# Performance work log

Hardware: AMD Instinct MI355X
Metric: run time of the kernel (lower is better)

The kernel has to match this reference:

```python
import jax, jax.numpy as jnp
import numpy as np

B, T, D = 2, 2048, 2048
N, K, H = 16, 8, 128            # heads, kv heads, head_dim
SOFT_CAP = 50.0
WINDOW = 1024
SCALE = H ** -0.5               # query_pre_attn_scalar
ROPE_BASE = 10000.0
ROPE_SCALE = 1.0
K_MASK = -2.3819763e+38


def rms_norm(x, scale, eps=1e-6):
    var = jnp.mean(jnp.square(x), axis=-1, keepdims=True)
    return x * jax.lax.rsqrt(var + eps) * (1.0 + scale)


def apply_rope(x, positions):
    # x: [B,T,heads,H]; positions: [B,T] int
    head_dim = x.shape[-1]
    fraction = 2.0 * jnp.arange(head_dim // 2, dtype=jnp.float32) / head_dim
    timescale = ROPE_BASE ** fraction                      # [H/2]
    sinusoid = positions[..., None].astype(jnp.float32) / timescale  # [B,T,H/2]
    sinusoid = sinusoid[..., None, :] / ROPE_SCALE          # [B,T,1,H/2]
    sin, cos = jnp.sin(sinusoid), jnp.cos(sinusoid)
    first, second = jnp.split(x, 2, axis=-1)
    return jnp.concatenate([first * cos - second * sin,
                            second * cos + first * sin], axis=-1)


def setup_inputs() -> dict:
    key = jax.random.key(0)
    ks = jax.random.split(key, 6)
    x = jax.random.normal(ks[0], (B, T, D), jnp.float32)
    q_w = jax.random.normal(ks[1], (N, D, H), jnp.float32) * (D ** -0.5)
    kv_w = jax.random.normal(ks[2], (2, K, D, H), jnp.float32) * (D ** -0.5)
    o_w = jax.random.normal(ks[3], (N, H, D), jnp.float32) * ((N * H) ** -0.5)
    qnorm_scale = 0.1 * jax.random.normal(ks[4], (H,), jnp.float32)
    knorm_scale = 0.1 * jax.random.normal(ks[5], (H,), jnp.float32)
    segment_pos = jnp.broadcast_to(jnp.arange(T, dtype=jnp.int32), (B, T))
    attn_mask = jnp.broadcast_to(jnp.tril(jnp.ones((T, T), dtype=bool)), (B, T, T))
    return {"x": x, "q_w": q_w, "kv_w": kv_w, "o_w": o_w,
            "qnorm_scale": qnorm_scale, "knorm_scale": knorm_scale,
            "segment_pos": segment_pos, "attn_mask": attn_mask}


def reference(x, q_w, kv_w, o_w, qnorm_scale, knorm_scale, segment_pos, attn_mask):
    # projections
    q = jnp.einsum('BTD,NDH->BTNH', x, q_w)            # [B,T,N,H]
    k = jnp.einsum('BSD,KDH->BSKH', x, kv_w[0])        # [B,T,K,H]
    v = jnp.einsum('BSD,KDH->BSKH', x, kv_w[1])
    # QK RMSNorm, then RoPE, then query scaling (matches source order)
    q = apply_rope(rms_norm(q, qnorm_scale), segment_pos) * SCALE
    k = apply_rope(rms_norm(k, knorm_scale), segment_pos)
    # GQA: regroup query heads per kv head
    G = N // K
    qg = q.reshape(B, T, K, G, H)
    logits = jnp.einsum('BTKGH,BSKH->BTKGS', qg, k).reshape(B, T, N, T)
    # logit soft cap
    logits = jnp.tanh(logits / SOFT_CAP) * SOFT_CAP
    # sliding window mask combined with causal attn_mask
    pos_q = segment_pos[:, :, None]
    pos_k = segment_pos[:, None, :]
    sliding = (pos_k > pos_q - WINDOW) & (pos_k < pos_q + WINDOW)
    mask = attn_mask & sliding                          # [B,T,S]
    padded = jnp.where(mask[:, :, None, :], logits, K_MASK)
    probs = jax.nn.softmax(padded, axis=-1).astype(k.dtype)
    enc = jnp.einsum('BTKGS,BSKH->BTKGH',
                     probs.reshape(B, T, K, G, T), v).reshape(B, T, N, H)
    return jnp.einsum('BTNH,NHD->BTD', enc, o_w)
```

## Files before the change

kernel.cpp:

```cpp
#include <hip/hip_runtime.h>
#include <stdint.h>

#define BB 2
#define TT 2048
#define DD 2048
#define NHD 16
#define KVH 8
#define HD 128
#define JC 4096
#define WIN 1024
#define SCALE_Q 0.08838834764831845f

typedef __attribute__((ext_vector_type(8))) short bf16x8;
typedef __attribute__((ext_vector_type(8))) unsigned short us8;
typedef __attribute__((ext_vector_type(4))) unsigned short us4;
typedef __attribute__((ext_vector_type(4))) float f32x4;
typedef __attribute__((ext_vector_type(16))) float f32x16;
typedef __attribute__((ext_vector_type(4))) unsigned int u32x4;

#define GAS __attribute__((address_space(1)))
#define LAS __attribute__((address_space(3)))

__device__ __forceinline__ unsigned short f2bf(float f) {
  unsigned u = __float_as_uint(f);
  u += 0x7FFFu + ((u >> 16) & 1u);
  return (unsigned short)(u >> 16);
}
__device__ __forceinline__ float bf2f(unsigned short u) {
  return __uint_as_float(((unsigned)u) << 16);
}

__device__ __forceinline__ void gload16(const void* g, void* l) {
  __builtin_amdgcn_global_load_lds((const GAS unsigned int*)g, (LAS unsigned int*)l, 16, 0, 0);
}

#define VMCNT(n) asm volatile("s_waitcnt vmcnt(" #n ")" ::: "memory")

__global__ void __launch_bounds__(256) k_pre(
    const float4* __restrict__ x4, us4* __restrict__ xb,
    const float* __restrict__ qw, const float* __restrict__ kvw,
    const float* __restrict__ ow, unsigned short* __restrict__ Wt,
    unsigned short* __restrict__ Wt_o) {
  __shared__ float tile[32][33];
  int id = blockIdx.x;
  int tid = threadIdx.x;
  if (id < 8192) {
    int i = id * 256 + tid;
    float4 v = x4[i];
    us4 o;
    o[0] = f2bf(v.x); o[1] = f2bf(v.y); o[2] = f2bf(v.z); o[3] = f2bf(v.w);
    xb[i] = o;
    return;
  }
  const float* ib;
  unsigned short* ob;
  int ldin, c0, r0;
  int t = id - 8192;
  if (t < 8192) {
    int bx = t & 3, by = (t >> 2) & 63, z = t >> 8;
    ib = (z < 16) ? qw + (long)z * 2048 * 128 : kvw + (long)(z - 16) * 2048 * 128;
    ob = Wt + (long)z * 128 * 2048;
    ldin = 128;
    c0 = bx * 32; r0 = by * 32;
  } else {
    int u = t - 8192;
    ib = ow; ob = Wt_o; ldin = 2048;
    c0 = (u & 63) * 32; r0 = (u >> 6) * 32;
  }
  int tx = tid & 31, ty = tid >> 5;
#pragma unroll
  for (int i = 0; i < 4; i++)
    tile[ty + i * 8][tx] = ib[(long)(r0 + ty + i * 8) * ldin + c0 + tx];
  __syncthreads();
#pragma unroll
  for (int i = 0; i < 4; i++)
    ob[(long)(c0 + ty + i * 8) * 2048 + r0 + tx] = f2bf(tile[tx][ty + i * 8]);
}

template <bool BF16OUT>
__global__ void __launch_bounds__(512, 2) k_gemm8p(
    const unsigned short* __restrict__ A, const unsigned short* __restrict__ Bt,
    void* __restrict__ Cv, int Nn, int nby) {
  constexpr int KD = 2048;
  constexpr int NT = KD / 64;
  __shared__ short lds[2 * 4 * 8192];

  int tid = threadIdx.x, lane = tid & 63, w = tid >> 6;
  int wm = w >> 2, wn = w & 3;
  int id = blockIdx.x;
  int cpx = gridDim.x >> 3;
  id = (id & 7) * cpx + (id >> 3);
  int m0 = (id / nby) * 256, n0 = (id % nby) * 256;

  int srow = tid >> 3;
  int scol = ((tid & 7) ^ ((tid >> 3) & 7)) * 8;
  const unsigned short* gA = A + (long)(m0 + srow) * KD + scol;
  const unsigned short* gB = Bt + (long)(n0 + srow) * KD + scol;
  int wrow = w * 8 * 64;

  auto STG = [&](int p, int ko, int r) {
    const unsigned short* gsrc = (r < 2) ? gA + (long)(r * 128) * KD + ko
                                         : gB + (long)((r - 2) * 128) * KD + ko;
    short* dst = &lds[p * 32768 + r * 8192 + wrow];
#pragma unroll
    for (int i = 0; i < 2; ++i)
      gload16(gsrc + (long)(i * 64) * KD, dst + i * 4096);
  };

  int c0 = ((lane >> 4) ^ (lane & 7)) * 8;
  int abase = wm * 8192 + (lane & 15) * 64;
  int bbase = 16384 + (wn >> 1) * 8192 + ((wn & 1) * 64 + (lane & 15)) * 64;

  f32x4 acc[8][4] = {};
#pragma unroll
  for (int r = 0; r < 4; ++r) STG(0, 0, r);
  STG(1, 64, 2);
  STG(1, 64, 3);
  VMCNT(4);
  __builtin_amdgcn_s_barrier();

  bf16x8 bf[4][2];
  for (int t = 0; t < NT; ++t) {
    const short* bp = &lds[(t & 1) * 32768];
    int sb1 = (t + 1) & 1, sb2 = t & 1;
    int ko1 = (t + 1) * 64, ko2 = (t + 2) * 64;
    bool s1 = (t + 1) < NT, s2 = (t + 2) < NT;
#pragma unroll
    for (int q = 0; q < 4; ++q) {
      bf16x8 af[2][2];
#pragma unroll
      for (int m2 = 0; m2 < 2; ++m2)
#pragma unroll
        for (int kk = 0; kk < 2; ++kk)
          af[m2][kk] = *(const bf16x8*)&bp[abase + (q * 2 + m2) * 16 * 64 + (c0 ^ (kk * 32))];
      if (q == 0) {
#pragma unroll
        for (int ni = 0; ni < 4; ++ni)
#pragma unroll
          for (int kk = 0; kk < 2; ++kk)
            bf[ni][kk] = *(const bf16x8*)&bp[bbase + ni * 16 * 64 + (c0 ^ (kk * 32))];
      }
      if (q == 0) { if (s1) STG(sb1, ko1, 0); }
      else if (q == 1) { if (s1) STG(sb1, ko1, 1); }
      else if (q == 2) { if (s2) STG(sb2, ko2, 2); }
      else {
        if (s2) { STG(sb2, ko2, 3); VMCNT(4); }
        else if (s1) VMCNT(0);
      }
      __builtin_amdgcn_s_barrier();
      asm volatile("s_waitcnt lgkmcnt(0)" ::: "memory");
      __builtin_amdgcn_sched_barrier(0);
      __builtin_amdgcn_s_setprio(1);
#pragma unroll
      for (int m2 = 0; m2 < 2; ++m2)
#pragma unroll
        for (int ni = 0; ni < 4; ++ni)
#pragma unroll
          for (int kk = 0; kk < 2; ++kk)
            acc[q * 2 + m2][ni] = __builtin_amdgcn_mfma_f32_16x16x32_bf16(
                af[m2][kk], bf[ni][kk], acc[q * 2 + m2][ni], 0, 0, 0);
      __builtin_amdgcn_s_setprio(0);
      __builtin_amdgcn_s_barrier();
    }
  }

#pragma unroll
  for (int mi = 0; mi < 8; mi++)
#pragma unroll
    for (int ni = 0; ni < 4; ni++)
#pragma unroll
      for (int r = 0; r < 4; r++) {
        int row = m0 + wm * 128 + mi * 16 + (lane >> 4) * 4 + r;
        int col = n0 + wn * 64 + ni * 16 + (lane & 15);
        if constexpr (BF16OUT)
          ((unsigned short*)Cv)[(long)row * Nn + col] = f2bf(acc[mi][ni][r]);
        else
          ((float*)Cv)[(long)row * Nn + col] = acc[mi][ni][r];
      }
}

template <int BM, int BN, int NWN, int THREADS, int NBUF, bool BF16OUT>
__global__ void __launch_bounds__(THREADS, 2) k_gemm9(
    const unsigned short* __restrict__ A, const unsigned short* __restrict__ Bt,
    void* __restrict__ Cv, int M, int Nn, int nby) {
  constexpr int KD = 2048;
  constexpr int NT = KD / 32;
  constexpr int ROWS = BM + BN;
  constexpr int RPI = THREADS / 4;
  constexpr int IA = BM / RPI;
  constexpr int IPT = ROWS / RPI;
  constexpr int MT = BM / 32;
  constexpr int MT2 = MT / 2;
  __shared__ short lds[NBUF][ROWS * 32];

  int tid = threadIdx.x, lane = tid & 63, w = tid >> 6;
  int wm = w / NWN, wn = w % NWN;
  int id = blockIdx.x;
  int cpx = gridDim.x >> 3;
  id = (id & 7) * cpx + (id >> 3);
  int m0 = (id / nby) * BM, n0 = (id % nby) * BN;

  int srow = tid >> 2;
  int scol = ((tid & 3) ^ ((tid >> 3) & 3)) * 8;
  const unsigned short* gA = A + (long)(m0 + srow) * KD + scol;
  const unsigned short* gB = Bt + (long)(n0 + srow) * KD + scol;

  auto STG = [&](int p, int ko, int j) {
    if (j < IA)
      gload16(gA + (long)j * RPI * KD + ko, &lds[p][(j * RPI + w * 16) * 32]);
    else
      gload16(gB + (long)(j - IA) * RPI * KD + ko,
              &lds[p][(BM + (j - IA) * RPI + w * 16) * 32]);
  };

  int frag = (lane & 15) * 32 + (((lane >> 4) ^ ((lane >> 1) & 3)) * 8);
  int abase = wm * (BM / 2) * 32 + frag;
  int bbase = (BM + wn * 64) * 32 + frag;

  f32x4 acc[MT][4] = {};
#pragma unroll
  for (int tt = 0; tt < NBUF - 1; ++tt)
#pragma unroll
    for (int j = 0; j < IPT; ++j) STG(tt, tt * 32, j);
  {
    constexpr int PW = IPT * (NBUF - 2);
    if constexpr (PW >= 8)      VMCNT(8);
    else if constexpr (PW == 6) VMCNT(6);
    else if constexpr (PW == 4) VMCNT(4);
    else                        VMCNT(0);
  }
  __builtin_amdgcn_s_barrier();

  int buf = 0, sp = NBUF - 1;
  for (int t = 0; t < NT; ++t) {
    const short* bufp = lds[buf];
    bool st = (t + NBUF - 1) < NT;
    int ko = (t + NBUF - 1) * 32;
    bf16x8 bfr[4], af[MT2];
#pragma unroll
    for (int ni = 0; ni < 4; ++ni)
      bfr[ni] = *(const bf16x8*)&bufp[bbase + ni * 16 * 32];
#pragma unroll
    for (int mi = 0; mi < MT2; ++mi)
      af[mi] = *(const bf16x8*)&bufp[abase + mi * 16 * 32];
    if (st) {
#pragma unroll
      for (int j = 0; j < IPT / 2; ++j) STG(sp, ko, j);
    }
    __builtin_amdgcn_s_barrier();
    asm volatile("s_waitcnt lgkmcnt(0)" ::: "memory");
    __builtin_amdgcn_sched_barrier(0);
    __builtin_amdgcn_s_setprio(1);
#pragma unroll
    for (int mi = 0; mi < MT2; ++mi)
#pragma unroll
      for (int ni = 0; ni < 4; ++ni)
        acc[mi][ni] = __builtin_amdgcn_mfma_f32_16x16x32_bf16(af[mi], bfr[ni], acc[mi][ni], 0, 0, 0);
    __builtin_amdgcn_s_setprio(0);
    __builtin_amdgcn_s_barrier();
    bf16x8 af2[MT2];
#pragma unroll
    for (int mi = 0; mi < MT2; ++mi)
      af2[mi] = *(const bf16x8*)&bufp[abase + (MT2 + mi) * 16 * 32];
    if (st) {
#pragma unroll
      for (int j = IPT / 2; j < IPT; ++j) STG(sp, ko, j);
    }
    {
      int rem = NT - 2 - t;
      if (rem > NBUF - 2) rem = NBUF - 2;
      if (rem == 2) {
        if constexpr (IPT == 4) VMCNT(8); else VMCNT(12);
      } else if (rem == 1) {
        if constexpr (IPT == 4) VMCNT(4); else VMCNT(6);
      } else if (rem == 0) {
        VMCNT(0);
      }
    }
    __builtin_amdgcn_s_barrier();
    asm volatile("s_waitcnt lgkmcnt(0)" ::: "memory");
    __builtin_amdgcn_sched_barrier(0);
    __builtin_amdgcn_s_setprio(1);
#pragma unroll
    for (int mi = 0; mi < MT2; ++mi)
#pragma unroll
      for (int ni = 0; ni < 4; ++ni)
        acc[MT2 + mi][ni] = __builtin_amdgcn_mfma_f32_16x16x32_bf16(af2[mi], bfr[ni], acc[MT2 + mi][ni], 0, 0, 0);
    __builtin_amdgcn_s_setprio(0);
    __builtin_amdgcn_s_barrier();
    buf = (buf == NBUF - 1) ? 0 : buf + 1;
    sp = (sp == NBUF - 1) ? 0 : sp + 1;
  }

#pragma unroll
  for (int mi = 0; mi < MT; mi++)
#pragma unroll
    for (int ni = 0; ni < 4; ni++)
#pragma unroll
      for (int r = 0; r < 4; r++) {
        int row = m0 + wm * (BM / 2) + mi * 16 + (lane >> 4) * 4 + r;
        int col = n0 + wn * 64 + ni * 16 + (lane & 15);
        if constexpr (BF16OUT)
          ((unsigned short*)Cv)[(long)row * Nn + col] = f2bf(acc[mi][ni][r]);
        else
          ((float*)Cv)[(long)row * Nn + col] = acc[mi][ni][r];
      }
}

__global__ void __launch_bounds__(256) k_post(
    const unsigned short* __restrict__ qkv, const float* __restrict__ qns,
    const float* __restrict__ kns, unsigned short* __restrict__ qb,
    unsigned short* __restrict__ kb, unsigned short* __restrict__ vbT) {
  int id = blockIdx.x;
  int tid = threadIdx.x;
  if (id < 24576) {
    int wid = tid >> 6, lane = tid & 63;
    long r = (long)id * 4 + wid;
    int b = (int)(r / (TT * 24));
    int rem = (int)(r % (TT * 24));
    int t = rem / 24, hd = rem % 24;
    const unsigned short* row = qkv + (long)(b * TT + t) * JC + (hd < 16 ? hd * HD : 2048 + (hd - 16) * HD);
    float f0 = bf2f(row[lane]), f1 = bf2f(row[lane + 64]);
    float ss = f0 * f0 + f1 * f1;
#pragma unroll
    for (int m = 1; m < 64; m <<= 1) ss += __shfl_xor(ss, m, 64);
    float rinv = rsqrtf(ss * (1.0f / 128.0f) + 1e-6f);
    const float* sc = (hd < 16) ? qns : kns;
    float y0 = f0 * rinv * (1.0f + sc[lane]);
    float y1 = f1 * rinv * (1.0f + sc[lane + 64]);
    float ts = exp2f((float)lane * (13.287712379549449f / 64.0f));
    float ang = (float)t / ts;
    float s, c;
    sincosf(ang, &s, &c);
    float o0 = y0 * c - y1 * s;
    float o1 = y1 * c + y0 * s;
    unsigned short* dst;
    if (hd < 16) {
      o0 *= SCALE_Q; o1 *= SCALE_Q;
      dst = qb + ((long)(b * NHD + hd) * TT + t) * HD;
    } else {
      dst = kb + ((long)(b * KVH + (hd - 16)) * TT + t) * HD;
    }
    dst[lane] = f2bf(o0);
    dst[lane + 64] = f2bf(o1);
    return;
  }
  __shared__ unsigned short tile[32][33];
  int t4 = id - 24576;
  int bx = t4 & 3, by = (t4 >> 2) & 63, z = t4 >> 8;
  const unsigned short* ib = qkv + 3072 + (long)(z / 8) * 2048 * 4096 + (long)(z % 8) * 128;
  unsigned short* ob = vbT + (long)z * 128 * 2048;
  int c0 = bx * 32, r0 = by * 32;
  int tx = tid & 31, ty = tid >> 5;
#pragma unroll
  for (int i = 0; i < 4; i++)
    tile[ty + i * 8][tx] = ib[(long)(r0 + ty + i * 8) * 4096 + c0 + tx];
  __syncthreads();
#pragma unroll
  for (int i = 0; i < 4; i++)
    ob[(long)(c0 + ty + i * 8) * 2048 + r0 + tx] = tile[tx][ty + i * 8];
}

template <bool FULL>
__device__ __forceinline__ void softcap16(const f32x16& s16, float* pr, float& lsum,
                                          int s_base, int tq, int g) {
#pragma unroll
  for (int r = 0; r < 16; r++) {
    float x = s16[r];
    float e2 = __builtin_amdgcn_exp2f(0.05770780163555853f * x);
    float p = __builtin_amdgcn_exp2f(-144.26950408889634f * __builtin_amdgcn_rcpf(1.0f + e2));
    if (!FULL) {
      int s = s_base + (r & 3) + 8 * (r >> 2) + 4 * g;
      bool valid = (s <= tq) && (s > tq - WIN);
      p = valid ? p : 0.0f;
    }
    lsum += p;
    pr[r] = p;
  }
}

__device__ __forceinline__ void hswap(unsigned& a, unsigned& b, int g) {
  unsigned ax = (unsigned)__shfl_xor((int)a, 32, 64);
  unsigned bx = (unsigned)__shfl_xor((int)b, 32, 64);
  unsigned r0 = g ? bx : a;
  unsigned r1 = g ? b : ax;
  a = r0; b = r1;
}

__global__ void __launch_bounds__(256, 2) k_attn(
    const unsigned short* __restrict__ qb, const unsigned short* __restrict__ kb,
    const unsigned short* __restrict__ vbT, unsigned short* __restrict__ enc) {
  __shared__ short Kl[2][64][128];
  __shared__ short Vt[2][128][64];
  int tid = threadIdx.x, lane = tid & 63, w = tid >> 6;
  int g = lane >> 5, l31 = lane & 31;
  int id = blockIdx.x;
  int b = id >> 8;
  int rem = id & 255;
  int n = rem >> 4;
  int traw = rem & 15;
  int tile = b ? ((traw + 8) & 15) : traw;
  int t0 = tile * 128;
  int kh = n >> 1;
  const unsigned short* qbase = qb + ((long)(b * NHD + n) * TT + t0 + w * 32) * HD;
  const unsigned short* kbase = kb + (long)(b * KVH + kh) * TT * HD;
  const unsigned short* vbase = vbT + (long)(b * KVH + kh) * HD * TT;

  bf16x8 bq[8];
  {
    const unsigned short* qp = qbase + (long)l31 * HD + g * 8;
#pragma unroll
    for (int kb8 = 0; kb8 < 8; kb8++)
      bq[kb8] = *(const bf16x8*)(qp + kb8 * 16);
  }

  f32x16 acc[4] = {};
  float lsum = 0.0f;
  int t0w = t0 + w * 32;
  int tq = t0w + l31;
  int s_begin = (t0 >= WIN) ? t0 - WIN : 0;
  int s_end = t0 + 128;

  auto STAGE = [&](int buf, int s0) {
#pragma unroll
    for (int i = 0; i < 4; i++) {
      int row = w * 16 + i * 4 + (lane >> 4);
      int c16 = (lane & 15) ^ (row & 7);
      gload16(kbase + (long)(s0 + row) * HD + c16 * 8, &Kl[buf][w * 16 + i * 4][0]);
    }
#pragma unroll
    for (int i = 0; i < 4; i++) {
      int row = w * 32 + i * 8 + (lane >> 3);
      int c16 = (lane & 7) ^ (row & 7);
      gload16(vbase + (long)row * TT + s0 + c16 * 8, &Vt[buf][w * 32 + i * 8][0]);
    }
  };

  STAGE(0, s_begin);
  int cur = 0;
  for (int s0 = s_begin; s0 < s_end; s0 += 64) {
    bool more = (s0 + 64 < s_end);
    if (more) {
      STAGE(cur ^ 1, s0 + 64);
      VMCNT(8);
    } else {
      VMCNT(0);
    }
    __builtin_amdgcn_s_barrier();
    bool live = (s0 <= t0w + 31) && (s0 + 63 >= t0w - (WIN - 1));
    if (live) {
      f32x16 sc2[2] = {};
#pragma unroll
      for (int sb = 0; sb < 2; sb++) {
        int srow = sb * 32 + l31;
#pragma unroll
        for (int kb8 = 0; kb8 < 8; kb8++) {
          bf16x8 ak = *(const bf16x8*)&Kl[cur][srow][8 * ((2 * kb8 + g) ^ (srow & 7))];
          sc2[sb] = __builtin_amdgcn_mfma_f32_32x32x16_bf16(ak, bq[kb8], sc2[sb], 0, 0, 0);
        }
      }
      bool full = (s0 + 63 <= t0w) && (s0 >= t0w + 31 - (WIN - 1));
      unsigned pw[4][4];
#pragma unroll
      for (int sb = 0; sb < 2; sb++) {
        float pr[16];
        if (full) softcap16<true>(sc2[sb], pr, lsum, 0, tq, g);
        else      softcap16<false>(sc2[sb], pr, lsum, s0 + sb * 32, tq, g);
        unsigned X[4], Y[4];
#pragma unroll
        for (int m = 0; m < 4; m++) {
          asm("v_cvt_pk_bf16_f32 %0, %1, %2" : "=v"(X[m]) : "v"(pr[4 * m]), "v"(pr[4 * m + 1]));
          asm("v_cvt_pk_bf16_f32 %0, %1, %2" : "=v"(Y[m]) : "v"(pr[4 * m + 2]), "v"(pr[4 * m + 3]));
        }
#pragma unroll
        for (int kl = 0; kl < 2; kl++) {
          hswap(X[2 * kl], X[2 * kl + 1], g);
          hswap(Y[2 * kl], Y[2 * kl + 1], g);
          pw[sb * 2 + kl][0] = X[2 * kl];
          pw[sb * 2 + kl][1] = Y[2 * kl];
          pw[sb * 2 + kl][2] = X[2 * kl + 1];
          pw[sb * 2 + kl][3] = Y[2 * kl + 1];
        }
      }
#pragma unroll
      for (int ks = 0; ks < 4; ks++) {
        u32x4 t4 = {pw[ks][0], pw[ks][1], pw[ks][2], pw[ks][3]};
        bf16x8 pb = __builtin_bit_cast(bf16x8, t4);
#pragma unroll
        for (int ht = 0; ht < 4; ht++) {
          int hrow = ht * 32 + l31;
          bf16x8 av = *(const bf16x8*)&Vt[cur][hrow][8 * ((2 * ks + g) ^ (hrow & 7))];
          acc[ht] = __builtin_amdgcn_mfma_f32_32x32x16_bf16(av, pb, acc[ht], 0, 0, 0);
        }
      }
    }
    asm volatile("s_waitcnt lgkmcnt(0)" ::: "memory");
    __builtin_amdgcn_s_barrier();
    cur ^= 1;
  }

  lsum += __shfl_xor(lsum, 32, 64);
  float inv = __builtin_amdgcn_rcpf(lsum);
  unsigned short* dst = enc + ((long)(b * TT + tq) * NHD + n) * HD;
#pragma unroll
  for (int ht = 0; ht < 4; ht++)
#pragma unroll
    for (int r4 = 0; r4 < 4; r4++) {
      us4 o;
#pragma unroll
      for (int e = 0; e < 4; e++) o[e] = f2bf(acc[ht][r4 * 4 + e] * inv);
      *(us4*)(dst + ht * 32 + 8 * r4 + 4 * g) = o;
    }
}

extern "C" void kernel_launch(void* const* d_in, const int* in_sizes, int n_in,
                              void* d_out, int out_size, void* d_ws, size_t ws_size,
                              hipStream_t stream) {
  const float* x    = (const float*)d_in[0];
  const float* q_w  = (const float*)d_in[1];
  const float* kv_w = (const float*)d_in[2];
  const float* o_w  = (const float*)d_in[3];
  const float* qns  = (const float*)d_in[4];
  const float* kns  = (const float*)d_in[5];

  if (ws_size < (104ull << 20)) return;
  char* ws = (char*)d_ws;
  unsigned short* qkvb = (unsigned short*)(ws + 0);
  unsigned short* enc  = (unsigned short*)(ws + 0);
  unsigned short* x_bf = (unsigned short*)(ws + (64ll << 20));
  unsigned short* qb   = (unsigned short*)(ws + (64ll << 20));
  unsigned short* Wt   = (unsigned short*)(ws + (80ll << 20));
  unsigned short* kb   = (unsigned short*)(ws + (80ll << 20));
  unsigned short* vbT  = (unsigned short*)(ws + (88ll << 20));
  unsigned short* Wt_o = (unsigned short*)(ws + (96ll << 20));

  k_pre<<<20480, 256, 0, stream>>>((const float4*)x, (us4*)x_bf, q_w, kv_w, o_w, Wt, Wt_o);
  k_gemm8p<true><<<256, 512, 0, stream>>>(x_bf, Wt, qkvb, 4096, 16);
  k_post<<<28672, 256, 0, stream>>>(qkvb, qns, kns, qb, kb, vbT);
  k_attn<<<512, 256, 0, stream>>>(qb, kb, vbT, enc);
  k_gemm9<128, 128, 2, 256, 3, false><<<512, 256, 0, stream>>>(enc, Wt_o, (float*)d_out, 4096, 2048, 16);
}
```

Measured before the change: 210.1 us.

## Split long-window attention tiles across two blocks with atomic-counter merge

Query tiles with long key ranges (tiles 4-15) are split into two key-range segments handled by separate blocks, growing the grid from 512 to 896 blocks. Each segment writes its unnormalized bf16 partial output and row sums to workspace. The second block to finish, detected via an atomic counter zeroed in the pre-kernel, adds both partials, normalizes and writes the final output. This balances per-block work and raises occupancy, at the cost of extra global traffic, fences, and an extra bf16 rounding of partials.

After: 443.0 us. +110.8%, slower.

```diff
diff --git a/kernel.cpp b/kernel.cpp
--- a/kernel.cpp
+++ b/kernel.cpp
@@ -40,10 +40,11 @@
     const float4* __restrict__ x4, us4* __restrict__ xb,
     const float* __restrict__ qw, const float* __restrict__ kvw,
     const float* __restrict__ ow, unsigned short* __restrict__ Wt,
-    unsigned short* __restrict__ Wt_o) {
+    unsigned short* __restrict__ Wt_o, int* __restrict__ pcnt) {
   __shared__ float tile[32][33];
   int id = blockIdx.x;
   int tid = threadIdx.x;
+  if (id == 0 && tid < 384) pcnt[tid] = 0;
   if (id < 8192) {
     int i = id * 256 + tid;
     float4 v = x4[i];
@@ -389,19 +390,31 @@
 
 __global__ void __launch_bounds__(256, 2) k_attn(
     const unsigned short* __restrict__ qb, const unsigned short* __restrict__ kb,
-    const unsigned short* __restrict__ vbT, unsigned short* __restrict__ enc) {
+    const unsigned short* __restrict__ vbT, unsigned short* __restrict__ enc,
+    unsigned short* __restrict__ ppart, float* __restrict__ plsum,
+    int* __restrict__ pcnt) {
   __shared__ short Kl[2][64][128];
   __shared__ short Vt[2][128][64];
+  __shared__ int sflag;
   int tid = threadIdx.x, lane = tid & 63, w = tid >> 6;
   int g = lane >> 5, l31 = lane & 31;
   int id = blockIdx.x;
-  int b = id >> 8;
-  int rem = id & 255;
-  int n = rem >> 4;
-  int traw = rem & 15;
-  int tile = b ? ((traw + 8) & 15) : traw;
+  int combo = id / 28;
+  int s28 = id % 28;
+  int b = combo >> 4, n = combo & 15;
+  int tile, seg, nseg;
+  if (s28 < 4) { tile = s28; seg = 0; nseg = 1; }
+  else { int u = s28 - 4; tile = 4 + (u >> 1); seg = u & 1; nseg = 2; }
   int t0 = tile * 128;
   int kh = n >> 1;
+  int sb0 = (t0 >= WIN) ? t0 - WIN : 0;
+  int NTt = (t0 + 128 - sb0) >> 6;
+  int NT1 = (NTt + 1) >> 1;
+  int gs0, gs_end;
+  if (nseg == 1)      { gs0 = sb0;             gs_end = t0 + 128; }
+  else if (seg == 0)  { gs0 = sb0;             gs_end = sb0 + NT1 * 64; }
+  else                { gs0 = sb0 + NT1 * 64;  gs_end = t0 + 128; }
+
   const unsigned short* qbase = qb + ((long)(b * NHD + n) * TT + t0 + w * 32) * HD;
   const unsigned short* kbase = kb + (long)(b * KVH + kh) * TT * HD;
   const unsigned short* vbase = vbT + (long)(b * KVH + kh) * HD * TT;
@@ -418,8 +431,6 @@
   float lsum = 0.0f;
   int t0w = t0 + w * 32;
   int tq = t0w + l31;
-  int s_begin = (t0 >= WIN) ? t0 - WIN : 0;
-  int s_end = t0 + 128;
 
   auto STAGE = [&](int buf, int s0) {
 #pragma unroll
@@ -436,10 +447,10 @@
     }
   };
 
-  STAGE(0, s_begin);
+  STAGE(0, gs0);
   int cur = 0;
-  for (int s0 = s_begin; s0 < s_end; s0 += 64) {
-    bool more = (s0 + 64 < s_end);
+  for (int s0 = gs0; s0 < gs_end; s0 += 64) {
+    bool more = (s0 + 64 < gs_end);
     if (more) {
       STAGE(cur ^ 1, s0 + 64);
       VMCNT(8);
@@ -500,6 +511,49 @@
   }
 
   lsum += __shfl_xor(lsum, 32, 64);
+  int qrel = w * 32 + l31;
+
+  if (nseg == 2) {
+    int pidx = combo * 12 + (tile - 4);
+    unsigned short* myp = ppart + ((long)(pidx * 2 + seg)) * 16384;
+    float* myl = plsum + (pidx * 2 + seg) * 128;
+#pragma unroll
+    for (int ht = 0; ht < 4; ht++)
+#pragma unroll
+      for (int r4 = 0; r4 < 4; r4++) {
+        us4 o;
+#pragma unroll
+        for (int e = 0; e < 4; e++) o[e] = f2bf(acc[ht][r4 * 4 + e]);
+        *(us4*)(myp + qrel * 128 + ht * 32 + 8 * r4 + 4 * g) = o;
+      }
+    if (g == 0) myl[qrel] = lsum;
+    __threadfence();
+    __syncthreads();
+    if (tid == 0) sflag = atomicAdd(&pcnt[pidx], 1);
+    __syncthreads();
+    if (sflag == 0) return;
+    __threadfence();
+    const unsigned short* pp = ppart + ((long)(pidx * 2 + (seg ^ 1))) * 16384;
+    const float* plp = plsum + (pidx * 2 + (seg ^ 1)) * 128;
+    float ltot = lsum + plp[qrel];
+    float inv = __builtin_amdgcn_rcpf(ltot);
+    unsigned short* dst = enc + ((long)(b * TT + t0 + qrel) * NHD + n) * HD;
+#pragma unroll
+    for (int ht = 0; ht < 4; ht++)
+#pragma unroll
+      for (int r4 = 0; r4 < 4; r4++) {
+        us4 pv = *(const us4*)(pp + qrel * 128 + ht * 32 + 8 * r4 + 4 * g);
+        us4 o;
+#pragma unroll
+        for (int e = 0; e < 4; e++) {
+          float own = bf2f(f2bf(acc[ht][r4 * 4 + e]));
+          o[e] = f2bf((own + bf2f(pv[e])) * inv);
+        }
+        *(us4*)(dst + ht * 32 + 8 * r4 + 4 * g) = o;
+      }
+    return;
+  }
+
   float inv = __builtin_amdgcn_rcpf(lsum);
   unsigned short* dst = enc + ((long)(b * TT + tq) * NHD + n) * HD;
 #pragma unroll
@@ -525,18 +579,21 @@
 
   if (ws_size < (104ull << 20)) return;
   char* ws = (char*)d_ws;
-  unsigned short* qkvb = (unsigned short*)(ws + 0);
-  unsigned short* enc  = (unsigned short*)(ws + 0);
-  unsigned short* x_bf = (unsigned short*)(ws + (64ll << 20));
-  unsigned short* qb   = (unsigned short*)(ws + (64ll << 20));
-  unsigned short* Wt   = (unsigned short*)(ws + (80ll << 20));
-  unsigned short* kb   = (unsigned short*)(ws + (80ll << 20));
-  unsigned short* vbT  = (unsigned short*)(ws + (88ll << 20));
-  unsigned short* Wt_o = (unsigned short*)(ws + (96ll << 20));
-
-  k_pre<<<20480, 256, 0, stream>>>((const float4*)x, (us4*)x_bf, q_w, kv_w, o_w, Wt, Wt_o);
+  unsigned short* qkvb  = (unsigned short*)(ws + 0);
+  unsigned short* ppart = (unsigned short*)(ws + 0);
+  float*          plsum = (float*)(ws + (24ll << 20));
+  unsigned short* enc   = (unsigned short*)(ws + (32ll << 20));
+  int*            pcnt  = (int*)(ws + (48ll << 20));
+  unsigned short* x_bf  = (unsigned short*)(ws + (64ll << 20));
+  unsigned short* qb    = (unsigned short*)(ws + (64ll << 20));
+  unsigned short* Wt    = (unsigned short*)(ws + (80ll << 20));
+  unsigned short* kb    = (unsigned short*)(ws + (80ll << 20));
+  unsigned short* vbT   = (unsigned short*)(ws + (88ll << 20));
+  unsigned short* Wt_o  = (unsigned short*)(ws + (96ll << 20));
+
+  k_pre<<<20480, 256, 0, stream>>>((const float4*)x, (us4*)x_bf, q_w, kv_w, o_w, Wt, Wt_o, pcnt);
   k_gemm8p<true><<<256, 512, 0, stream>>>(x_bf, Wt, qkvb, 4096, 16);
   k_post<<<28672, 256, 0, stream>>>(qkvb, qns, kns, qb, kb, vbT);
-  k_attn<<<512, 256, 0, stream>>>(qb, kb, vbT, enc);
+  k_attn<<<896, 256, 0, stream>>>(qb, kb, vbT, enc, ppart, plsum, pcnt);
   k_gemm9<128, 128, 2, 256, 3, false><<<512, 256, 0, stream>>>(enc, Wt_o, (float*)d_out, 4096, 2048, 16);
 }
```
